# Performance work log

Hardware: AMD Instinct MI355X
Metric: run time of the kernel (lower is better)

Reference implementation:

```python
import jax, jax.numpy as jnp
import numpy as np

INPUT, HIDDEN, C, H, W, PK = 64, 128, 16, 32, 32, 4
B, T = 512, 1024

def hardsigmoid(v):
    return jnp.clip(v / 6.0 + 0.5, 0.0, 1.0)

def setup_inputs() -> dict:
    key = jax.random.key(0)
    ks = jax.random.split(key, 9)
    s_rnn = 1.0 / np.sqrt(HIDDEN)
    s_map = 1.0 / np.sqrt(HIDDEN)
    return {
        "x": jax.random.normal(ks[0], (B, T, INPUT), dtype=jnp.float32),
        "W_ih": jax.random.uniform(ks[1], (HIDDEN, INPUT), minval=-s_rnn, maxval=s_rnn),
        "b_ih": jax.random.uniform(ks[2], (HIDDEN,), minval=-s_rnn, maxval=s_rnn),
        "W_hh": jax.random.uniform(ks[3], (HIDDEN, HIDDEN), minval=-s_rnn, maxval=s_rnn),
        "b_hh": jax.random.uniform(ks[4], (HIDDEN,), minval=-s_rnn, maxval=s_rnn),
        "W_gate": jax.random.uniform(ks[5], (HIDDEN, HIDDEN), minval=-s_rnn, maxval=s_rnn),
        "b_gate": jax.random.uniform(ks[6], (HIDDEN,), minval=-s_rnn, maxval=s_rnn),
        "W_map": jax.random.uniform(ks[7], (C * H * W, HIDDEN), minval=-s_map, maxval=s_map),
        "b_map": jax.random.uniform(ks[8], (C * H * W,), minval=-s_map, maxval=s_map),
    }

def reference(x, W_ih, b_ih, W_hh, b_hh, W_gate, b_gate, W_map, b_map):
    batch, seq_len, _ = x.shape
    h0 = jnp.zeros((batch, HIDDEN), dtype=x.dtype)
    agg0 = jnp.zeros((batch, HIDDEN), dtype=x.dtype)

    def step(carry, xt):
        h, agg = carry
        h = jnp.tanh(xt @ W_ih.T + b_ih + h @ W_hh.T + b_hh)
        gate = hardsigmoid(h @ W_gate.T + b_gate)
        return (h, agg + h * gate), None

    (h, agg), _ = jax.lax.scan(step, (h0, agg0), jnp.swapaxes(x, 0, 1))
    agg = agg / float(seq_len)

    mapped = (agg @ W_map.T + b_map).reshape(batch, C, H, W)
    # AvgPool2d(kernel=PK, stride=PK) via reshape-mean
    pooled = mapped.reshape(batch, C, H // PK, PK, W // PK, PK).mean(axis=(3, 5))
    upsampled = jnp.repeat(jnp.repeat(pooled, PK, axis=2), PK, axis=3)
    return mapped * hardsigmoid(upsampled)
```

## Files before the change

kernel.cpp:

```cpp
#include <hip/hip_runtime.h>
#include <hip/hip_bf16.h>

#define T_SEQ 1024
#define BATCH 512
#define INPUT 64
#define HID   128

typedef __attribute__((ext_vector_type(8))) short bf16x8;
typedef __attribute__((ext_vector_type(4))) short s16x4;
typedef __attribute__((ext_vector_type(4))) float f32x4;
typedef __attribute__((ext_vector_type(2))) unsigned int u32x2;

#define MFMA __builtin_amdgcn_mfma_f32_16x16x32_bf16

__device__ __forceinline__ short f2bf(float f) {
    union { float f; unsigned u; } v; v.f = f;
    unsigned r = (v.u + 0x7FFFu + ((v.u >> 16) & 1u)) >> 16;
    return (short)r;
}

__device__ __forceinline__ unsigned cvtpk_bf16(float lo, float hi) {
    unsigned r;
    asm("v_cvt_pk_bf16_f32 %0, %1, %2" : "=v"(r) : "v"(lo), "v"(hi));
    return r;
}

__device__ __forceinline__ float fast_tanh(float s) {
    float e = __expf(2.0f * s);
    return 1.0f - 2.0f * __builtin_amdgcn_rcpf(e + 1.0f);
}

__device__ __forceinline__ float hsig(float v) {
    return __builtin_amdgcn_fmed3f(v * 0.16666666666666666f + 0.5f, 0.0f, 1.0f);
}

__device__ __forceinline__ void wg_barrier_lds() {
    asm volatile("s_waitcnt lgkmcnt(0)" ::: "memory");
    __builtin_amdgcn_s_barrier();
    asm volatile("" ::: "memory");
}

__global__ __launch_bounds__(256) void cvt_kernel(const float* __restrict__ in,
                                                  short* __restrict__ out, int n4) {
    int i = blockIdx.x * 256 + threadIdx.x;
    if (i >= n4) return;
    f32x4 v = ((const f32x4*)in)[i];
    s16x4 o;
    #pragma unroll
    for (int j = 0; j < 4; ++j) o[j] = f2bf(v[j]);
    ((s16x4*)out)[i] = o;
}

template<bool PRE>
__global__ __launch_bounds__(512, 2) void rnn_kernel(
    const float* __restrict__ xf_, const short* __restrict__ xb,
    const float* __restrict__ W_ih, const float* __restrict__ b_ih,
    const float* __restrict__ W_hh, const float* __restrict__ b_hh,
    const float* __restrict__ W_gate, const float* __restrict__ b_gate,
    float* __restrict__ agg_out)
{
    __shared__ __align__(16) short sh[2][16][136];

    const int tid  = threadIdx.x;
    const int wave = tid >> 6, lane = tid & 63;
    const int q = lane >> 4, l15 = lane & 15;
    const int b0 = blockIdx.x * 16;
    const int group = wave >> 2;
    const int gw = wave & 3;
    const int R0 = 32 * gw, R1 = R0 + 16;

    bf16x8 wih[2][2], whh[2][4], wgf[2][4];
    #pragma unroll
    for (int tile = 0; tile < 2; ++tile) {
        const int row = (tile ? R1 : R0) + l15;
        #pragma unroll
        for (int f = 0; f < 2; ++f) {
            const float* p = W_ih + row * INPUT + f * 32 + q * 8;
            bf16x8 v;
            #pragma unroll
            for (int j = 0; j < 8; ++j) v[j] = f2bf(p[j]);
            wih[tile][f] = v;
        }
        #pragma unroll
        for (int f = 0; f < 4; ++f) {
            const float* p = W_hh + row * HID + f * 32 + q * 8;
            bf16x8 v;
            #pragma unroll
            for (int j = 0; j < 8; ++j) v[j] = f2bf(p[j]);
            whh[tile][f] = v;
        }
        #pragma unroll
        for (int f = 0; f < 4; ++f) {
            const float* p = W_gate + row * HID + f * 32 + q * 8;
            bf16x8 v;
            #pragma unroll
            for (int j = 0; j < 8; ++j) v[j] = f2bf(p[j]);
            wgf[tile][f] = v;
        }
    }

    f32x4 bias1[2], biasg[2], zero4;
    #pragma unroll
    for (int tile = 0; tile < 2; ++tile) {
        const int rbase = (tile ? R1 : R0) + q * 4;
        #pragma unroll
        for (int r = 0; r < 4; ++r) {
            bias1[tile][r] = b_ih[rbase + r] + b_hh[rbase + r];
            biasg[tile][r] = b_gate[rbase + r];
        }
    }
    #pragma unroll
    for (int r = 0; r < 4; ++r) zero4[r] = 0.0f;

    f32x4 agg0 = zero4, agg1 = zero4;
    f32x4 hpA = zero4, hpB = zero4;
    f32x4 accx0, accx1;
    bf16x8 xf0, xf1;

    const long lanebase = ((long)(b0 + l15) * T_SEQ) * INPUT + q * 8;
    const short* xb_lane = PRE ? (xb + lanebase) : nullptr;
    const float* xf_lane = PRE ? nullptr : (xf_ + lanebase);

    auto load_x = [&](int tt) {
        if constexpr (PRE) {
            const short* p = xb_lane + (long)tt * INPUT;
            xf0 = *(const bf16x8*)p;
            xf1 = *(const bf16x8*)(p + 32);
        } else {
            const float* p = xf_lane + (long)tt * INPUT;
            f32x4 a0 = *(const f32x4*)p,        a1 = *(const f32x4*)(p + 4);
            f32x4 a2 = *(const f32x4*)(p + 32), a3 = *(const f32x4*)(p + 36);
            #pragma unroll
            for (int j = 0; j < 4; ++j) {
                xf0[j] = f2bf(a0[j]); xf0[4 + j] = f2bf(a1[j]);
                xf1[j] = f2bf(a2[j]); xf1[4 + j] = f2bf(a3[j]);
            }
        }
    };

    auto critical = [&](int t) {
        const int rb = (t & 1) ^ 1, wb = t & 1;
        bf16x8 hf0 = *(const bf16x8*)&sh[rb][l15][q * 8];
        bf16x8 hf1 = *(const bf16x8*)&sh[rb][l15][32 + q * 8];
        bf16x8 hf2 = *(const bf16x8*)&sh[rb][l15][64 + q * 8];
        bf16x8 hf3 = *(const bf16x8*)&sh[rb][l15][96 + q * 8];
        f32x4 a0 = MFMA(whh[0][0], hf0, accx0, 0, 0, 0);
        f32x4 c0 = MFMA(whh[0][2], hf2, zero4, 0, 0, 0);
        f32x4 a1 = MFMA(whh[1][0], hf0, accx1, 0, 0, 0);
        f32x4 c1 = MFMA(whh[1][2], hf2, zero4, 0, 0, 0);
        a0 = MFMA(whh[0][1], hf1, a0, 0, 0, 0);
        c0 = MFMA(whh[0][3], hf3, c0, 0, 0, 0);
        a1 = MFMA(whh[1][1], hf1, a1, 0, 0, 0);
        c1 = MFMA(whh[1][3], hf3, c1, 0, 0, 0);
        int tt = t + 2; if (tt > T_SEQ - 1) tt = T_SEQ - 1;
        load_x(tt);
        hpA[0] = fast_tanh(a0[0] + c0[0]);
        hpA[1] = fast_tanh(a0[1] + c0[1]);
        hpA[2] = fast_tanh(a0[2] + c0[2]);
        hpA[3] = fast_tanh(a0[3] + c0[3]);
        hpB[0] = fast_tanh(a1[0] + c1[0]);
        hpB[1] = fast_tanh(a1[1] + c1[1]);
        hpB[2] = fast_tanh(a1[2] + c1[2]);
        hpB[3] = fast_tanh(a1[3] + c1[3]);
        u32x2 p0, p1;
        p0[0] = cvtpk_bf16(hpA[0], hpA[1]); p0[1] = cvtpk_bf16(hpA[2], hpA[3]);
        p1[0] = cvtpk_bf16(hpB[0], hpB[1]); p1[1] = cvtpk_bf16(hpB[2], hpB[3]);
        *(u32x2*)&sh[wb][l15][R0 + q * 4] = p0;
        *(u32x2*)&sh[wb][l15][R1 + q * 4] = p1;
    };

    auto shadow = [&](int t) {
        const int rb = (t & 1) ^ 1;
        bf16x8 gf0 = *(const bf16x8*)&sh[rb][l15][q * 8];
        bf16x8 gf1 = *(const bf16x8*)&sh[rb][l15][32 + q * 8];
        bf16x8 gf2 = *(const bf16x8*)&sh[rb][l15][64 + q * 8];
        bf16x8 gf3 = *(const bf16x8*)&sh[rb][l15][96 + q * 8];
        f32x4 g0 = MFMA(wgf[0][0], gf0, biasg[0], 0, 0, 0);
        f32x4 e0 = MFMA(wgf[0][2], gf2, zero4, 0, 0, 0);
        f32x4 g1 = MFMA(wgf[1][0], gf0, biasg[1], 0, 0, 0);
        f32x4 e1 = MFMA(wgf[1][2], gf2, zero4, 0, 0, 0);
        g0 = MFMA(wgf[0][1], gf1, g0, 0, 0, 0);
        e0 = MFMA(wgf[0][3], gf3, e0, 0, 0, 0);
        g1 = MFMA(wgf[1][1], gf1, g1, 0, 0, 0);
        e1 = MFMA(wgf[1][3], gf3, e1, 0, 0, 0);
        accx0 = MFMA(wih[0][0], xf0, bias1[0], 0, 0, 0);
        accx1 = MFMA(wih[1][0], xf0, bias1[1], 0, 0, 0);
        accx0 = MFMA(wih[0][1], xf1, accx0, 0, 0, 0);
        accx1 = MFMA(wih[1][1], xf1, accx1, 0, 0, 0);
        #pragma unroll
        for (int r = 0; r < 4; ++r) {
            agg0[r] += hpA[r] * hsig(g0[r] + e0[r]);
            agg1[r] += hpB[r] * hsig(g1[r] + e1[r]);
        }
    };

    load_x(group);
    accx0 = MFMA(wih[0][0], xf0, bias1[0], 0, 0, 0);
    accx1 = MFMA(wih[1][0], xf0, bias1[1], 0, 0, 0);
    accx0 = MFMA(wih[0][1], xf1, accx0, 0, 0, 0);
    accx1 = MFMA(wih[1][1], xf1, accx1, 0, 0, 0);
    if (group == 0) {
        hpA[0] = fast_tanh(accx0[0]); hpA[1] = fast_tanh(accx0[1]);
        hpA[2] = fast_tanh(accx0[2]); hpA[3] = fast_tanh(accx0[3]);
        hpB[0] = fast_tanh(accx1[0]); hpB[1] = fast_tanh(accx1[1]);
        hpB[2] = fast_tanh(accx1[2]); hpB[3] = fast_tanh(accx1[3]);
        u32x2 p0, p1;
        p0[0] = cvtpk_bf16(hpA[0], hpA[1]); p0[1] = cvtpk_bf16(hpA[2], hpA[3]);
        p1[0] = cvtpk_bf16(hpB[0], hpB[1]); p1[1] = cvtpk_bf16(hpB[2], hpB[3]);
        *(u32x2*)&sh[0][l15][R0 + q * 4] = p0;
        *(u32x2*)&sh[0][l15][R1 + q * 4] = p1;
        load_x(2);
    }
    wg_barrier_lds();

    if (group == 0) {
        for (int i = 0; i < 511; ++i) {
            shadow(2 * i + 1);   wg_barrier_lds();
            critical(2 * i + 2); wg_barrier_lds();
        }
        shadow(1023); wg_barrier_lds();
    } else {
        for (int i = 0; i < 511; ++i) {
            critical(2 * i + 1); wg_barrier_lds();
            shadow(2 * i + 2);   wg_barrier_lds();
        }
        critical(1023); wg_barrier_lds();
    }

    if (group == 1) {
        bf16x8 gf0 = *(const bf16x8*)&sh[1][l15][q * 8];
        bf16x8 gf1 = *(const bf16x8*)&sh[1][l15][32 + q * 8];
        bf16x8 gf2 = *(const bf16x8*)&sh[1][l15][64 + q * 8];
        bf16x8 gf3 = *(const bf16x8*)&sh[1][l15][96 + q * 8];
        f32x4 g0 = MFMA(wgf[0][0], gf0, biasg[0], 0, 0, 0);
        f32x4 e0 = MFMA(wgf[0][2], gf2, zero4, 0, 0, 0);
        f32x4 g1 = MFMA(wgf[1][0], gf0, biasg[1], 0, 0, 0);
        f32x4 e1 = MFMA(wgf[1][2], gf2, zero4, 0, 0, 0);
        g0 = MFMA(wgf[0][1], gf1, g0, 0, 0, 0);
        e0 = MFMA(wgf[0][3], gf3, e0, 0, 0, 0);
        g1 = MFMA(wgf[1][1], gf1, g1, 0, 0, 0);
        e1 = MFMA(wgf[1][3], gf3, e1, 0, 0, 0);
        #pragma unroll
        for (int r = 0; r < 4; ++r) {
            agg0[r] += hpA[r] * hsig(g0[r] + e0[r]);
            agg1[r] += hpB[r] * hsig(g1[r] + e1[r]);
        }
    }
    wg_barrier_lds();

    float* aggf = (float*)&sh[0][0][0];
    if (group == 0) {
        *(f32x4*)&aggf[l15 * HID + R0 + q * 4] = agg0;
        *(f32x4*)&aggf[l15 * HID + R1 + q * 4] = agg1;
    }
    wg_barrier_lds();
    if (group == 1) {
        const float s = 1.0f / (float)T_SEQ;
        f32x4 t0 = *(const f32x4*)&aggf[l15 * HID + R0 + q * 4];
        f32x4 t1 = *(const f32x4*)&aggf[l15 * HID + R1 + q * 4];
        #pragma unroll
        for (int r = 0; r < 4; ++r) { t0[r] = (t0[r] + agg0[r]) * s; t1[r] = (t1[r] + agg1[r]) * s; }
        *(f32x4*)&agg_out[(long)(b0 + l15) * HID + R0 + q * 4] = t0;
        *(f32x4*)&agg_out[(long)(b0 + l15) * HID + R1 + q * 4] = t1;
    }
}

template<bool PRE>
__global__ __launch_bounds__(256) void map_kernel(
    const float* __restrict__ agg, const float* __restrict__ Wf,
    const short* __restrict__ Wb, const float* __restrict__ b_map,
    float* __restrict__ mapped)
{
    const int tid  = threadIdx.x;
    const int wave = tid >> 6, lane = tid & 63;
    const int q = lane >> 4, l15 = lane & 15;
    const int mb = blockIdx.x & 31;
    const int nb = blockIdx.x >> 5;
    const int b0 = mb * 16;
    const int n0 = nb * 128 + wave * 32;

    bf16x8 af[4];
    #pragma unroll
    for (int kb = 0; kb < 4; ++kb) {
        const float* p = agg + (b0 + l15) * HID + kb * 32 + q * 8;
        bf16x8 f;
        #pragma unroll
        for (int j = 0; j < 8; ++j) f[j] = f2bf(p[j]);
        af[kb] = f;
    }
    #pragma unroll
    for (int tn = 0; tn < 2; ++tn) {
        int nn = n0 + tn * 16 + l15;
        float bias = b_map[nn];
        f32x4 c;
        #pragma unroll
        for (int r = 0; r < 4; ++r) c[r] = bias;
        #pragma unroll
        for (int kb = 0; kb < 4; ++kb) {
            bf16x8 f;
            if (PRE) {
                f = *(const bf16x8*)(Wb + (long)nn * HID + kb * 32 + q * 8);
            } else {
                const float* p = Wf + (long)nn * HID + kb * 32 + q * 8;
                #pragma unroll
                for (int j = 0; j < 8; ++j) f[j] = f2bf(p[j]);
            }
            c = __builtin_amdgcn_mfma_f32_16x16x32_bf16(af[kb], f, c, 0, 0, 0);
        }
        #pragma unroll
        for (int r = 0; r < 4; ++r)
            mapped[(long)(b0 + q * 4 + r) * 16384 + nn] = c[r];
    }
}

__global__ __launch_bounds__(256) void pool_gate_kernel(float* __restrict__ mapped)
{
    __shared__ float sh_part[256];
    __shared__ float sh_gate[64];
    const int tid = threadIdx.x;
    float* plane = mapped + (long)blockIdx.x * 1024;

    f32x4 m4 = *(const f32x4*)(plane + tid * 4);
    sh_part[tid] = m4[0] + m4[1] + m4[2] + m4[3];
    __syncthreads();
    if (tid < 64) {
        int ph = tid >> 3, pw = tid & 7;
        float s = 0.0f;
        #pragma unroll
        for (int i = 0; i < 4; ++i) s += sh_part[(4 * ph + i) * 8 + pw];
        sh_gate[tid] = hsig(s * (1.0f / 16.0f));
    }
    __syncthreads();
    int h = tid >> 3, wb = tid & 7;
    float g = sh_gate[(h >> 2) * 8 + wb];
    f32x4 o = m4 * g;
    *(f32x4*)(plane + tid * 4) = o;
}

extern "C" void kernel_launch(void* const* d_in, const int* in_sizes, int n_in,
                              void* d_out, int out_size, void* d_ws, size_t ws_size,
                              hipStream_t stream) {
    const float* x      = (const float*)d_in[0];
    const float* W_ih   = (const float*)d_in[1];
    const float* b_ih   = (const float*)d_in[2];
    const float* W_hh   = (const float*)d_in[3];
    const float* b_hh   = (const float*)d_in[4];
    const float* W_gate = (const float*)d_in[5];
    const float* b_gate = (const float*)d_in[6];
    const float* W_map  = (const float*)d_in[7];
    const float* b_map  = (const float*)d_in[8];
    float* out = (float*)d_out;

    const size_t xb_bytes = (size_t)BATCH * T_SEQ * INPUT * 2;
    const size_t wm_bytes = (size_t)16384 * HID * 2;
    const size_t agg_bytes = (size_t)BATCH * HID * 4;
    const bool pre = ws_size >= xb_bytes + wm_bytes + agg_bytes;

    if (pre) {
        short* x_bf  = (short*)d_ws;
        short* wm_bf = (short*)((char*)d_ws + xb_bytes);
        float* agg   = (float*)((char*)d_ws + xb_bytes + wm_bytes);

        cvt_kernel<<<(BATCH * T_SEQ * INPUT / 4 + 255) / 256, 256, 0, stream>>>(x, x_bf, BATCH * T_SEQ * INPUT / 4);
        cvt_kernel<<<(16384 * HID / 4 + 255) / 256, 256, 0, stream>>>(W_map, wm_bf, 16384 * HID / 4);
        rnn_kernel<true><<<32, 512, 0, stream>>>(x, x_bf, W_ih, b_ih, W_hh, b_hh,
                                                 W_gate, b_gate, agg);
        map_kernel<true><<<4096, 256, 0, stream>>>(agg, W_map, wm_bf, b_map, out);
    } else {
        float* agg = (float*)d_ws;
        rnn_kernel<false><<<32, 512, 0, stream>>>(x, nullptr, W_ih, b_ih, W_hh, b_hh,
                                                  W_gate, b_gate, agg);
        map_kernel<false><<<4096, 256, 0, stream>>>(agg, W_map, nullptr, b_map, out);
    }
    pool_gate_kernel<<<BATCH * 16, 256, 0, stream>>>(out);
}
```

Measured before the change: 694.7 us.

## Merge RNN wave groups into one 256-thread block with software-pipelined gate and input

Before, the RNN kernel used two 4-wave groups that alternated critical (recurrent) and shadow (gate/input projection) phases with a barrier between each phase. Now a single 4-wave group does every step. Each step reads h once and issues the recurrent, gate and next-input MFMAs together. Gate application is delayed one step and x is prefetched three steps ahead. The goal is to halve barriers per timestep, drop the cross-group LDS reduction, and let independent MFMAs fill the latency of the serial tanh chain. The cost is more MFMA and VALU work on the critical path per wave, since the gate matmul no longer runs in a separate group.

After: 718.4 us. 1.03x slower.

```diff
diff --git a/kernel.cpp b/kernel.cpp
--- a/kernel.cpp
+++ b/kernel.cpp
@@ -52,7 +52,7 @@
 }
 
 template<bool PRE>
-__global__ __launch_bounds__(512, 2) void rnn_kernel(
+__global__ __launch_bounds__(256) void rnn_kernel(
     const float* __restrict__ xf_, const short* __restrict__ xb,
     const float* __restrict__ W_ih, const float* __restrict__ b_ih,
     const float* __restrict__ W_hh, const float* __restrict__ b_hh,
@@ -65,9 +65,7 @@
     const int wave = tid >> 6, lane = tid & 63;
     const int q = lane >> 4, l15 = lane & 15;
     const int b0 = blockIdx.x * 16;
-    const int group = wave >> 2;
-    const int gw = wave & 3;
-    const int R0 = 32 * gw, R1 = R0 + 16;
+    const int R0 = 32 * wave, R1 = R0 + 16;
 
     bf16x8 wih[2][2], whh[2][4], wgf[2][4];
     #pragma unroll
@@ -113,156 +111,145 @@
     for (int r = 0; r < 4; ++r) zero4[r] = 0.0f;
 
     f32x4 agg0 = zero4, agg1 = zero4;
-    f32x4 hpA = zero4, hpB = zero4;
-    f32x4 accx0, accx1;
-    bf16x8 xf0, xf1;
+    f32x4 hp1_0 = zero4, hp1_1 = zero4;
+    f32x4 hp2_0 = zero4, hp2_1 = zero4;
+    f32x4 gat0 = zero4, gat1 = zero4;
+    f32x4 axA0, axA1, axB0, axB1;
+    bf16x8 xB0a, xB0b, xB1a, xB1b;
 
     const long lanebase = ((long)(b0 + l15) * T_SEQ) * INPUT + q * 8;
     const short* xb_lane = PRE ? (xb + lanebase) : nullptr;
     const float* xf_lane = PRE ? nullptr : (xf_ + lanebase);
 
-    auto load_x = [&](int tt) {
+    auto load_pair = [&](int tt, bf16x8& fa, bf16x8& fb) {
         if constexpr (PRE) {
             const short* p = xb_lane + (long)tt * INPUT;
-            xf0 = *(const bf16x8*)p;
-            xf1 = *(const bf16x8*)(p + 32);
+            fa = *(const bf16x8*)p;
+            fb = *(const bf16x8*)(p + 32);
         } else {
             const float* p = xf_lane + (long)tt * INPUT;
             f32x4 a0 = *(const f32x4*)p,        a1 = *(const f32x4*)(p + 4);
             f32x4 a2 = *(const f32x4*)(p + 32), a3 = *(const f32x4*)(p + 36);
             #pragma unroll
             for (int j = 0; j < 4; ++j) {
-                xf0[j] = f2bf(a0[j]); xf0[4 + j] = f2bf(a1[j]);
-                xf1[j] = f2bf(a2[j]); xf1[4 + j] = f2bf(a3[j]);
+                fa[j] = f2bf(a0[j]); fa[4 + j] = f2bf(a1[j]);
+                fb[j] = f2bf(a2[j]); fb[4 + j] = f2bf(a3[j]);
             }
         }
     };
 
-    auto critical = [&](int t) {
+    auto step = [&](int t, f32x4& axM0, f32x4& axM1, f32x4& axS0, f32x4& axS1,
+                    bf16x8& xfa, bf16x8& xfb) {
         const int rb = (t & 1) ^ 1, wb = t & 1;
         bf16x8 hf0 = *(const bf16x8*)&sh[rb][l15][q * 8];
         bf16x8 hf1 = *(const bf16x8*)&sh[rb][l15][32 + q * 8];
         bf16x8 hf2 = *(const bf16x8*)&sh[rb][l15][64 + q * 8];
         bf16x8 hf3 = *(const bf16x8*)&sh[rb][l15][96 + q * 8];
-        f32x4 a0 = MFMA(whh[0][0], hf0, accx0, 0, 0, 0);
+        #pragma unroll
+        for (int r = 0; r < 4; ++r) {
+            agg0[r] += hp2_0[r] * hsig(gat0[r]);
+            agg1[r] += hp2_1[r] * hsig(gat1[r]);
+        }
+        axS0 = MFMA(wih[0][0], xfa, bias1[0], 0, 0, 0);
+        axS1 = MFMA(wih[1][0], xfa, bias1[1], 0, 0, 0);
+        axS0 = MFMA(wih[0][1], xfb, axS0, 0, 0, 0);
+        axS1 = MFMA(wih[1][1], xfb, axS1, 0, 0, 0);
+        int tt = t + 3; if (tt > T_SEQ - 1) tt = T_SEQ - 1;
+        load_pair(tt, xfa, xfb);
+        f32x4 a0 = MFMA(whh[0][0], hf0, axM0, 0, 0, 0);
         f32x4 c0 = MFMA(whh[0][2], hf2, zero4, 0, 0, 0);
-        f32x4 a1 = MFMA(whh[1][0], hf0, accx1, 0, 0, 0);
+        f32x4 a1 = MFMA(whh[1][0], hf0, axM1, 0, 0, 0);
         f32x4 c1 = MFMA(whh[1][2], hf2, zero4, 0, 0, 0);
         a0 = MFMA(whh[0][1], hf1, a0, 0, 0, 0);
         c0 = MFMA(whh[0][3], hf3, c0, 0, 0, 0);
         a1 = MFMA(whh[1][1], hf1, a1, 0, 0, 0);
         c1 = MFMA(whh[1][3], hf3, c1, 0, 0, 0);
-        int tt = t + 2; if (tt > T_SEQ - 1) tt = T_SEQ - 1;
-        load_x(tt);
-        hpA[0] = fast_tanh(a0[0] + c0[0]);
-        hpA[1] = fast_tanh(a0[1] + c0[1]);
-        hpA[2] = fast_tanh(a0[2] + c0[2]);
-        hpA[3] = fast_tanh(a0[3] + c0[3]);
-        hpB[0] = fast_tanh(a1[0] + c1[0]);
-        hpB[1] = fast_tanh(a1[1] + c1[1]);
-        hpB[2] = fast_tanh(a1[2] + c1[2]);
-        hpB[3] = fast_tanh(a1[3] + c1[3]);
+        gat0 = MFMA(wgf[0][0], hf0, biasg[0], 0, 0, 0);
+        gat0 = MFMA(wgf[0][1], hf1, gat0, 0, 0, 0);
+        gat0 = MFMA(wgf[0][2], hf2, gat0, 0, 0, 0);
+        gat0 = MFMA(wgf[0][3], hf3, gat0, 0, 0, 0);
+        gat1 = MFMA(wgf[1][0], hf0, biasg[1], 0, 0, 0);
+        gat1 = MFMA(wgf[1][1], hf1, gat1, 0, 0, 0);
+        gat1 = MFMA(wgf[1][2], hf2, gat1, 0, 0, 0);
+        gat1 = MFMA(wgf[1][3], hf3, gat1, 0, 0, 0);
+        hp2_0 = hp1_0; hp2_1 = hp1_1;
+        hp1_0[0] = fast_tanh(a0[0] + c0[0]);
+        hp1_0[1] = fast_tanh(a0[1] + c0[1]);
+        hp1_0[2] = fast_tanh(a0[2] + c0[2]);
+        hp1_0[3] = fast_tanh(a0[3] + c0[3]);
+        hp1_1[0] = fast_tanh(a1[0] + c1[0]);
+        hp1_1[1] = fast_tanh(a1[1] + c1[1]);
+        hp1_1[2] = fast_tanh(a1[2] + c1[2]);
+        hp1_1[3] = fast_tanh(a1[3] + c1[3]);
         u32x2 p0, p1;
-        p0[0] = cvtpk_bf16(hpA[0], hpA[1]); p0[1] = cvtpk_bf16(hpA[2], hpA[3]);
-        p1[0] = cvtpk_bf16(hpB[0], hpB[1]); p1[1] = cvtpk_bf16(hpB[2], hpB[3]);
+        p0[0] = cvtpk_bf16(hp1_0[0], hp1_0[1]); p0[1] = cvtpk_bf16(hp1_0[2], hp1_0[3]);
+        p1[0] = cvtpk_bf16(hp1_1[0], hp1_1[1]); p1[1] = cvtpk_bf16(hp1_1[2], hp1_1[3]);
         *(u32x2*)&sh[wb][l15][R0 + q * 4] = p0;
         *(u32x2*)&sh[wb][l15][R1 + q * 4] = p1;
+        wg_barrier_lds();
     };
 
-    auto shadow = [&](int t) {
-        const int rb = (t & 1) ^ 1;
-        bf16x8 gf0 = *(const bf16x8*)&sh[rb][l15][q * 8];
-        bf16x8 gf1 = *(const bf16x8*)&sh[rb][l15][32 + q * 8];
-        bf16x8 gf2 = *(const bf16x8*)&sh[rb][l15][64 + q * 8];
-        bf16x8 gf3 = *(const bf16x8*)&sh[rb][l15][96 + q * 8];
-        f32x4 g0 = MFMA(wgf[0][0], gf0, biasg[0], 0, 0, 0);
-        f32x4 e0 = MFMA(wgf[0][2], gf2, zero4, 0, 0, 0);
-        f32x4 g1 = MFMA(wgf[1][0], gf0, biasg[1], 0, 0, 0);
-        f32x4 e1 = MFMA(wgf[1][2], gf2, zero4, 0, 0, 0);
-        g0 = MFMA(wgf[0][1], gf1, g0, 0, 0, 0);
-        e0 = MFMA(wgf[0][3], gf3, e0, 0, 0, 0);
-        g1 = MFMA(wgf[1][1], gf1, g1, 0, 0, 0);
-        e1 = MFMA(wgf[1][3], gf3, e1, 0, 0, 0);
-        accx0 = MFMA(wih[0][0], xf0, bias1[0], 0, 0, 0);
-        accx1 = MFMA(wih[1][0], xf0, bias1[1], 0, 0, 0);
-        accx0 = MFMA(wih[0][1], xf1, accx0, 0, 0, 0);
-        accx1 = MFMA(wih[1][1], xf1, accx1, 0, 0, 0);
-        #pragma unroll
-        for (int r = 0; r < 4; ++r) {
-            agg0[r] += hpA[r] * hsig(g0[r] + e0[r]);
-            agg1[r] += hpB[r] * hsig(g1[r] + e1[r]);
-        }
-    };
-
-    load_x(group);
-    accx0 = MFMA(wih[0][0], xf0, bias1[0], 0, 0, 0);
-    accx1 = MFMA(wih[1][0], xf0, bias1[1], 0, 0, 0);
-    accx0 = MFMA(wih[0][1], xf1, accx0, 0, 0, 0);
-    accx1 = MFMA(wih[1][1], xf1, accx1, 0, 0, 0);
-    if (group == 0) {
-        hpA[0] = fast_tanh(accx0[0]); hpA[1] = fast_tanh(accx0[1]);
-        hpA[2] = fast_tanh(accx0[2]); hpA[3] = fast_tanh(accx0[3]);
-        hpB[0] = fast_tanh(accx1[0]); hpB[1] = fast_tanh(accx1[1]);
-        hpB[2] = fast_tanh(accx1[2]); hpB[3] = fast_tanh(accx1[3]);
+    {
+        bf16x8 ta, tb;
+        load_pair(0, ta, tb);
+        axA0 = MFMA(wih[0][0], ta, bias1[0], 0, 0, 0);
+        axA1 = MFMA(wih[1][0], ta, bias1[1], 0, 0, 0);
+        axA0 = MFMA(wih[0][1], tb, axA0, 0, 0, 0);
+        axA1 = MFMA(wih[1][1], tb, axA1, 0, 0, 0);
+        hp1_0[0] = fast_tanh(axA0[0]); hp1_0[1] = fast_tanh(axA0[1]);
+        hp1_0[2] = fast_tanh(axA0[2]); hp1_0[3] = fast_tanh(axA0[3]);
+        hp1_1[0] = fast_tanh(axA1[0]); hp1_1[1] = fast_tanh(axA1[1]);
+        hp1_1[2] = fast_tanh(axA1[2]); hp1_1[3] = fast_tanh(axA1[3]);
         u32x2 p0, p1;
-        p0[0] = cvtpk_bf16(hpA[0], hpA[1]); p0[1] = cvtpk_bf16(hpA[2], hpA[3]);
-        p1[0] = cvtpk_bf16(hpB[0], hpB[1]); p1[1] = cvtpk_bf16(hpB[2], hpB[3]);
+        p0[0] = cvtpk_bf16(hp1_0[0], hp1_0[1]); p0[1] = cvtpk_bf16(hp1_0[2], hp1_0[3]);
+        p1[0] = cvtpk_bf16(hp1_1[0], hp1_1[1]); p1[1] = cvtpk_bf16(hp1_1[2], hp1_1[3]);
         *(u32x2*)&sh[0][l15][R0 + q * 4] = p0;
         *(u32x2*)&sh[0][l15][R1 + q * 4] = p1;
-        load_x(2);
-    }
-    wg_barrier_lds();
-
-    if (group == 0) {
-        for (int i = 0; i < 511; ++i) {
-            shadow(2 * i + 1);   wg_barrier_lds();
-            critical(2 * i + 2); wg_barrier_lds();
-        }
-        shadow(1023); wg_barrier_lds();
-    } else {
-        for (int i = 0; i < 511; ++i) {
-            critical(2 * i + 1); wg_barrier_lds();
-            shadow(2 * i + 2);   wg_barrier_lds();
-        }
-        critical(1023); wg_barrier_lds();
-    }
-
-    if (group == 1) {
-        bf16x8 gf0 = *(const bf16x8*)&sh[1][l15][q * 8];
-        bf16x8 gf1 = *(const bf16x8*)&sh[1][l15][32 + q * 8];
-        bf16x8 gf2 = *(const bf16x8*)&sh[1][l15][64 + q * 8];
-        bf16x8 gf3 = *(const bf16x8*)&sh[1][l15][96 + q * 8];
-        f32x4 g0 = MFMA(wgf[0][0], gf0, biasg[0], 0, 0, 0);
-        f32x4 e0 = MFMA(wgf[0][2], gf2, zero4, 0, 0, 0);
-        f32x4 g1 = MFMA(wgf[1][0], gf0, biasg[1], 0, 0, 0);
-        f32x4 e1 = MFMA(wgf[1][2], gf2, zero4, 0, 0, 0);
-        g0 = MFMA(wgf[0][1], gf1, g0, 0, 0, 0);
-        e0 = MFMA(wgf[0][3], gf3, e0, 0, 0, 0);
-        g1 = MFMA(wgf[1][1], gf1, g1, 0, 0, 0);
-        e1 = MFMA(wgf[1][3], gf3, e1, 0, 0, 0);
+        load_pair(1, ta, tb);
+        axA0 = MFMA(wih[0][0], ta, bias1[0], 0, 0, 0);
+        axA1 = MFMA(wih[1][0], ta, bias1[1], 0, 0, 0);
+        axA0 = MFMA(wih[0][1], tb, axA0, 0, 0, 0);
+        axA1 = MFMA(wih[1][1], tb, axA1, 0, 0, 0);
+        load_pair(2, xB0a, xB0b);
+        load_pair(3, xB1a, xB1b);
+        wg_barrier_lds();
+    }
+
+    for (int i = 0; i < 511; ++i) {
+        step(2 * i + 1, axA0, axA1, axB0, axB1, xB0a, xB0b);
+        step(2 * i + 2, axB0, axB1, axA0, axA1, xB1a, xB1b);
+    }
+    step(1023, axA0, axA1, axB0, axB1, xB0a, xB0b);
+
+    #pragma unroll
+    for (int r = 0; r < 4; ++r) {
+        agg0[r] += hp2_0[r] * hsig(gat0[r]);
+        agg1[r] += hp2_1[r] * hsig(gat1[r]);
+    }
+    {
+        bf16x8 hf0 = *(const bf16x8*)&sh[1][l15][q * 8];
+        bf16x8 hf1 = *(const bf16x8*)&sh[1][l15][32 + q * 8];
+        bf16x8 hf2 = *(const bf16x8*)&sh[1][l15][64 + q * 8];
+        bf16x8 hf3 = *(const bf16x8*)&sh[1][l15][96 + q * 8];
+        gat0 = MFMA(wgf[0][0], hf0, biasg[0], 0, 0, 0);
+        gat0 = MFMA(wgf[0][1], hf1, gat0, 0, 0, 0);
+        gat0 = MFMA(wgf[0][2], hf2, gat0, 0, 0, 0);
+        gat0 = MFMA(wgf[0][3], hf3, gat0, 0, 0, 0);
+        gat1 = MFMA(wgf[1][0], hf0, biasg[1], 0, 0, 0);
+        gat1 = MFMA(wgf[1][1], hf1, gat1, 0, 0, 0);
+        gat1 = MFMA(wgf[1][2], hf2, gat1, 0, 0, 0);
+        gat1 = MFMA(wgf[1][3], hf3, gat1, 0, 0, 0);
         #pragma unroll
         for (int r = 0; r < 4; ++r) {
-            agg0[r] += hpA[r] * hsig(g0[r] + e0[r]);
-            agg1[r] += hpB[r] * hsig(g1[r] + e1[r]);
-        }
-    }
-    wg_barrier_lds();
-
-    float* aggf = (float*)&sh[0][0][0];
-    if (group == 0) {
-        *(f32x4*)&aggf[l15 * HID + R0 + q * 4] = agg0;
-        *(f32x4*)&aggf[l15 * HID + R1 + q * 4] = agg1;
-    }
-    wg_barrier_lds();
-    if (group == 1) {
-        const float s = 1.0f / (float)T_SEQ;
-        f32x4 t0 = *(const f32x4*)&aggf[l15 * HID + R0 + q * 4];
-        f32x4 t1 = *(const f32x4*)&aggf[l15 * HID + R1 + q * 4];
-        #pragma unroll
-        for (int r = 0; r < 4; ++r) { t0[r] = (t0[r] + agg0[r]) * s; t1[r] = (t1[r] + agg1[r]) * s; }
-        *(f32x4*)&agg_out[(long)(b0 + l15) * HID + R0 + q * 4] = t0;
-        *(f32x4*)&agg_out[(long)(b0 + l15) * HID + R1 + q * 4] = t1;
-    }
+            agg0[r] += hp1_0[r] * hsig(gat0[r]);
+            agg1[r] += hp1_1[r] * hsig(gat1[r]);
+        }
+    }
+    const float s = 1.0f / (float)T_SEQ;
+    #pragma unroll
+    for (int r = 0; r < 4; ++r) { agg0[r] *= s; agg1[r] *= s; }
+    *(f32x4*)&agg_out[(long)(b0 + l15) * HID + R0 + q * 4] = agg0;
+    *(f32x4*)&agg_out[(long)(b0 + l15) * HID + R1 + q * 4] = agg1;
 }
 
 template<bool PRE>
@@ -363,12 +350,12 @@
 
         cvt_kernel<<<(BATCH * T_SEQ * INPUT / 4 + 255) / 256, 256, 0, stream>>>(x, x_bf, BATCH * T_SEQ * INPUT / 4);
         cvt_kernel<<<(16384 * HID / 4 + 255) / 256, 256, 0, stream>>>(W_map, wm_bf, 16384 * HID / 4);
-        rnn_kernel<true><<<32, 512, 0, stream>>>(x, x_bf, W_ih, b_ih, W_hh, b_hh,
+        rnn_kernel<true><<<32, 256, 0, stream>>>(x, x_bf, W_ih, b_ih, W_hh, b_hh,
                                                  W_gate, b_gate, agg);
         map_kernel<true><<<4096, 256, 0, stream>>>(agg, W_map, wm_bf, b_map, out);
     } else {
         float* agg = (float*)d_ws;
-        rnn_kernel<false><<<32, 512, 0, stream>>>(x, nullptr, W_ih, b_ih, W_hh, b_hh,
+        rnn_kernel<false><<<32, 256, 0, stream>>>(x, nullptr, W_ih, b_ih, W_hh, b_hh,
                                                   W_gate, b_gate, agg);
         map_kernel<false><<<4096, 256, 0, stream>>>(agg, W_map, nullptr, b_map, out);
     }
```

## Drop x bf16 pre-conversion, prefetch fp32 x deeper, fuse pool-gate into map kernel

Applied to the files above, without the earlier changes.

Removes the separate kernel that converted the full input sequence to bf16. The RNN kernel now loads fp32 x directly into a double-buffered register prefetch several steps ahead, converting it inside the shadow phase. It also folds the 4x4 average-pool and hardsigmoid gating into the map kernel using shuffles and shared memory, which eliminates the extra read and write pass over the output tensor. The cost is more registers (launch bounds changed to 1 block per SM) and in-loop conversion work on the recurrent path.

New measurement: 769.2 us. 10.7% more time.

```diff
diff --git a/kernel.cpp b/kernel.cpp
--- a/kernel.cpp
+++ b/kernel.cpp
@@ -51,9 +51,8 @@
     ((s16x4*)out)[i] = o;
 }
 
-template<bool PRE>
-__global__ __launch_bounds__(512, 2) void rnn_kernel(
-    const float* __restrict__ xf_, const short* __restrict__ xb,
+__global__ __launch_bounds__(512, 1) void rnn_kernel(
+    const float* __restrict__ xf_,
     const float* __restrict__ W_ih, const float* __restrict__ b_ih,
     const float* __restrict__ W_hh, const float* __restrict__ b_hh,
     const float* __restrict__ W_gate, const float* __restrict__ b_gate,
@@ -115,28 +114,9 @@
     f32x4 agg0 = zero4, agg1 = zero4;
     f32x4 hpA = zero4, hpB = zero4;
     f32x4 accx0, accx1;
-    bf16x8 xf0, xf1;
-
-    const long lanebase = ((long)(b0 + l15) * T_SEQ) * INPUT + q * 8;
-    const short* xb_lane = PRE ? (xb + lanebase) : nullptr;
-    const float* xf_lane = PRE ? nullptr : (xf_ + lanebase);
-
-    auto load_x = [&](int tt) {
-        if constexpr (PRE) {
-            const short* p = xb_lane + (long)tt * INPUT;
-            xf0 = *(const bf16x8*)p;
-            xf1 = *(const bf16x8*)(p + 32);
-        } else {
-            const float* p = xf_lane + (long)tt * INPUT;
-            f32x4 a0 = *(const f32x4*)p,        a1 = *(const f32x4*)(p + 4);
-            f32x4 a2 = *(const f32x4*)(p + 32), a3 = *(const f32x4*)(p + 36);
-            #pragma unroll
-            for (int j = 0; j < 4; ++j) {
-                xf0[j] = f2bf(a0[j]); xf0[4 + j] = f2bf(a1[j]);
-                xf1[j] = f2bf(a2[j]); xf1[4 + j] = f2bf(a3[j]);
-            }
-        }
-    };
+    f32x4 P0, P1, P2, P3, Q0, Q1, Q2, Q3;
+
+    const float* xf_lane = xf_ + ((long)(b0 + l15) * T_SEQ) * INPUT + q * 8;
 
     auto critical = [&](int t) {
         const int rb = (t & 1) ^ 1, wb = t & 1;
@@ -152,8 +132,6 @@
         c0 = MFMA(whh[0][3], hf3, c0, 0, 0, 0);
         a1 = MFMA(whh[1][1], hf1, a1, 0, 0, 0);
         c1 = MFMA(whh[1][3], hf3, c1, 0, 0, 0);
-        int tt = t + 2; if (tt > T_SEQ - 1) tt = T_SEQ - 1;
-        load_x(tt);
         hpA[0] = fast_tanh(a0[0] + c0[0]);
         hpA[1] = fast_tanh(a0[1] + c0[1]);
         hpA[2] = fast_tanh(a0[2] + c0[2]);
@@ -169,12 +147,28 @@
         *(u32x2*)&sh[wb][l15][R1 + q * 4] = p1;
     };
 
-    auto shadow = [&](int t) {
+    auto shadow = [&](int t, f32x4& r0, f32x4& r1, f32x4& r2, f32x4& r3) {
         const int rb = (t & 1) ^ 1;
         bf16x8 gf0 = *(const bf16x8*)&sh[rb][l15][q * 8];
         bf16x8 gf1 = *(const bf16x8*)&sh[rb][l15][32 + q * 8];
         bf16x8 gf2 = *(const bf16x8*)&sh[rb][l15][64 + q * 8];
         bf16x8 gf3 = *(const bf16x8*)&sh[rb][l15][96 + q * 8];
+        bf16x8 fa, fb;
+        #pragma unroll
+        for (int j = 0; j < 4; ++j) {
+            fa[j] = f2bf(r0[j]); fa[4 + j] = f2bf(r1[j]);
+            fb[j] = f2bf(r2[j]); fb[4 + j] = f2bf(r3[j]);
+        }
+        accx0 = MFMA(wih[0][0], fa, bias1[0], 0, 0, 0);
+        accx1 = MFMA(wih[1][0], fa, bias1[1], 0, 0, 0);
+        accx0 = MFMA(wih[0][1], fb, accx0, 0, 0, 0);
+        accx1 = MFMA(wih[1][1], fb, accx1, 0, 0, 0);
+        int tt = t + 5; if (tt > T_SEQ - 1) tt = T_SEQ - 1;
+        {
+            const float* p = xf_lane + (long)tt * INPUT;
+            r0 = *(const f32x4*)p;        r1 = *(const f32x4*)(p + 4);
+            r2 = *(const f32x4*)(p + 32); r3 = *(const f32x4*)(p + 36);
+        }
         f32x4 g0 = MFMA(wgf[0][0], gf0, biasg[0], 0, 0, 0);
         f32x4 e0 = MFMA(wgf[0][2], gf2, zero4, 0, 0, 0);
         f32x4 g1 = MFMA(wgf[1][0], gf0, biasg[1], 0, 0, 0);
@@ -183,10 +177,6 @@
         e0 = MFMA(wgf[0][3], gf3, e0, 0, 0, 0);
         g1 = MFMA(wgf[1][1], gf1, g1, 0, 0, 0);
         e1 = MFMA(wgf[1][3], gf3, e1, 0, 0, 0);
-        accx0 = MFMA(wih[0][0], xf0, bias1[0], 0, 0, 0);
-        accx1 = MFMA(wih[1][0], xf0, bias1[1], 0, 0, 0);
-        accx0 = MFMA(wih[0][1], xf1, accx0, 0, 0, 0);
-        accx1 = MFMA(wih[1][1], xf1, accx1, 0, 0, 0);
         #pragma unroll
         for (int r = 0; r < 4; ++r) {
             agg0[r] += hpA[r] * hsig(g0[r] + e0[r]);
@@ -194,35 +184,58 @@
         }
     };
 
-    load_x(group);
-    accx0 = MFMA(wih[0][0], xf0, bias1[0], 0, 0, 0);
-    accx1 = MFMA(wih[1][0], xf0, bias1[1], 0, 0, 0);
-    accx0 = MFMA(wih[0][1], xf1, accx0, 0, 0, 0);
-    accx1 = MFMA(wih[1][1], xf1, accx1, 0, 0, 0);
+    {
+        const float* p = xf_lane + (long)group * INPUT;
+        f32x4 a0 = *(const f32x4*)p,        a1 = *(const f32x4*)(p + 4);
+        f32x4 a2 = *(const f32x4*)(p + 32), a3 = *(const f32x4*)(p + 36);
+        bf16x8 ta, tb;
+        #pragma unroll
+        for (int j = 0; j < 4; ++j) {
+            ta[j] = f2bf(a0[j]); ta[4 + j] = f2bf(a1[j]);
+            tb[j] = f2bf(a2[j]); tb[4 + j] = f2bf(a3[j]);
+        }
+        accx0 = MFMA(wih[0][0], ta, bias1[0], 0, 0, 0);
+        accx1 = MFMA(wih[1][0], ta, bias1[1], 0, 0, 0);
+        accx0 = MFMA(wih[0][1], tb, accx0, 0, 0, 0);
+        accx1 = MFMA(wih[1][1], tb, accx1, 0, 0, 0);
+        if (group == 0) {
+            hpA[0] = fast_tanh(accx0[0]); hpA[1] = fast_tanh(accx0[1]);
+            hpA[2] = fast_tanh(accx0[2]); hpA[3] = fast_tanh(accx0[3]);
+            hpB[0] = fast_tanh(accx1[0]); hpB[1] = fast_tanh(accx1[1]);
+            hpB[2] = fast_tanh(accx1[2]); hpB[3] = fast_tanh(accx1[3]);
+            u32x2 p0, p1;
+            p0[0] = cvtpk_bf16(hpA[0], hpA[1]); p0[1] = cvtpk_bf16(hpA[2], hpA[3]);
+            p1[0] = cvtpk_bf16(hpB[0], hpB[1]); p1[1] = cvtpk_bf16(hpB[2], hpB[3]);
+            *(u32x2*)&sh[0][l15][R0 + q * 4] = p0;
+            *(u32x2*)&sh[0][l15][R1 + q * 4] = p1;
+        }
+        const float* pp = xf_lane + (long)(group ? 3 : 2) * INPUT;
+        P0 = *(const f32x4*)pp;        P1 = *(const f32x4*)(pp + 4);
+        P2 = *(const f32x4*)(pp + 32); P3 = *(const f32x4*)(pp + 36);
+        const float* pq = xf_lane + (long)(group ? 5 : 4) * INPUT;
+        Q0 = *(const f32x4*)pq;        Q1 = *(const f32x4*)(pq + 4);
+        Q2 = *(const f32x4*)(pq + 32); Q3 = *(const f32x4*)(pq + 36);
+    }
+    wg_barrier_lds();
+
     if (group == 0) {
-        hpA[0] = fast_tanh(accx0[0]); hpA[1] = fast_tanh(accx0[1]);
-        hpA[2] = fast_tanh(accx0[2]); hpA[3] = fast_tanh(accx0[3]);
-        hpB[0] = fast_tanh(accx1[0]); hpB[1] = fast_tanh(accx1[1]);
-        hpB[2] = fast_tanh(accx1[2]); hpB[3] = fast_tanh(accx1[3]);
-        u32x2 p0, p1;
-        p0[0] = cvtpk_bf16(hpA[0], hpA[1]); p0[1] = cvtpk_bf16(hpA[2], hpA[3]);
-        p1[0] = cvtpk_bf16(hpB[0], hpB[1]); p1[1] = cvtpk_bf16(hpB[2], hpB[3]);
-        *(u32x2*)&sh[0][l15][R0 + q * 4] = p0;
-        *(u32x2*)&sh[0][l15][R1 + q * 4] = p1;
-        load_x(2);
-    }
-    wg_barrier_lds();
-
-    if (group == 0) {
-        for (int i = 0; i < 511; ++i) {
-            shadow(2 * i + 1);   wg_barrier_lds();
-            critical(2 * i + 2); wg_barrier_lds();
-        }
-        shadow(1023); wg_barrier_lds();
+        shadow(1, P0, P1, P2, P3);   wg_barrier_lds();
+        critical(2);                 wg_barrier_lds();
+        for (int i = 0; i < 255; ++i) {
+            shadow(4 * i + 3, Q0, Q1, Q2, Q3); wg_barrier_lds();
+            critical(4 * i + 4);               wg_barrier_lds();
+            shadow(4 * i + 5, P0, P1, P2, P3); wg_barrier_lds();
+            critical(4 * i + 6);               wg_barrier_lds();
+        }
+        shadow(1023, Q0, Q1, Q2, Q3); wg_barrier_lds();
     } else {
-        for (int i = 0; i < 511; ++i) {
-            critical(2 * i + 1); wg_barrier_lds();
-            shadow(2 * i + 2);   wg_barrier_lds();
+        critical(1);                 wg_barrier_lds();
+        shadow(2, P0, P1, P2, P3);   wg_barrier_lds();
+        for (int i = 0; i < 255; ++i) {
+            critical(4 * i + 3);               wg_barrier_lds();
+            shadow(4 * i + 4, Q0, Q1, Q2, Q3); wg_barrier_lds();
+            critical(4 * i + 5);               wg_barrier_lds();
+            shadow(4 * i + 6, P0, P1, P2, P3); wg_barrier_lds();
         }
         critical(1023); wg_barrier_lds();
     }
@@ -269,8 +282,11 @@
 __global__ __launch_bounds__(256) void map_kernel(
     const float* __restrict__ agg, const float* __restrict__ Wf,
     const short* __restrict__ Wb, const float* __restrict__ b_map,
-    float* __restrict__ mapped)
+    float* __restrict__ out)
 {
+    __shared__ float sh_pool[4][16][8];
+    __shared__ float sh_gate[16][8];
+
     const int tid  = threadIdx.x;
     const int wave = tid >> 6, lane = tid & 63;
     const int q = lane >> 4, l15 = lane & 15;
@@ -288,6 +304,7 @@
         for (int j = 0; j < 8; ++j) f[j] = f2bf(p[j]);
         af[kb] = f;
     }
+    f32x4 cc[2];
     #pragma unroll
     for (int tn = 0; tn < 2; ++tn) {
         int nn = n0 + tn * 16 + l15;
@@ -307,34 +324,35 @@
             }
             c = __builtin_amdgcn_mfma_f32_16x16x32_bf16(af[kb], f, c, 0, 0, 0);
         }
+        cc[tn] = c;
+        f32x4 t = c;
+        #pragma unroll
+        for (int r = 0; r < 4; ++r) {
+            t[r] += __shfl_xor(t[r], 1);
+            t[r] += __shfl_xor(t[r], 2);
+        }
+        if ((l15 & 3) == 0) {
+            int pw = tn * 4 + (l15 >> 2);
+            #pragma unroll
+            for (int r = 0; r < 4; ++r) sh_pool[wave][q * 4 + r][pw] = t[r];
+        }
+    }
+    __syncthreads();
+    if (tid < 128) {
+        int b = tid >> 3, pw = tid & 7;
+        float s = sh_pool[0][b][pw] + sh_pool[1][b][pw] +
+                  sh_pool[2][b][pw] + sh_pool[3][b][pw];
+        sh_gate[b][pw] = hsig(s * (1.0f / 16.0f));
+    }
+    __syncthreads();
+    #pragma unroll
+    for (int tn = 0; tn < 2; ++tn) {
+        int nn = n0 + tn * 16 + l15;
+        int pw = tn * 4 + (l15 >> 2);
         #pragma unroll
         for (int r = 0; r < 4; ++r)
-            mapped[(long)(b0 + q * 4 + r) * 16384 + nn] = c[r];
-    }
-}
-
-__global__ __launch_bounds__(256) void pool_gate_kernel(float* __restrict__ mapped)
-{
-    __shared__ float sh_part[256];
-    __shared__ float sh_gate[64];
-    const int tid = threadIdx.x;
-    float* plane = mapped + (long)blockIdx.x * 1024;
-
-    f32x4 m4 = *(const f32x4*)(plane + tid * 4);
-    sh_part[tid] = m4[0] + m4[1] + m4[2] + m4[3];
-    __syncthreads();
-    if (tid < 64) {
-        int ph = tid >> 3, pw = tid & 7;
-        float s = 0.0f;
-        #pragma unroll
-        for (int i = 0; i < 4; ++i) s += sh_part[(4 * ph + i) * 8 + pw];
-        sh_gate[tid] = hsig(s * (1.0f / 16.0f));
-    }
-    __syncthreads();
-    int h = tid >> 3, wb = tid & 7;
-    float g = sh_gate[(h >> 2) * 8 + wb];
-    f32x4 o = m4 * g;
-    *(f32x4*)(plane + tid * 4) = o;
+            out[(long)(b0 + q * 4 + r) * 16384 + nn] = cc[tn][r] * sh_gate[q * 4 + r][pw];
+    }
 }
 
 extern "C" void kernel_launch(void* const* d_in, const int* in_sizes, int n_in,
@@ -351,26 +369,22 @@
     const float* b_map  = (const float*)d_in[8];
     float* out = (float*)d_out;
 
-    const size_t xb_bytes = (size_t)BATCH * T_SEQ * INPUT * 2;
     const size_t wm_bytes = (size_t)16384 * HID * 2;
     const size_t agg_bytes = (size_t)BATCH * HID * 4;
-    const bool pre = ws_size >= xb_bytes + wm_bytes + agg_bytes;
+    const bool pre = ws_size >= wm_bytes + agg_bytes;
 
     if (pre) {
-        short* x_bf  = (short*)d_ws;
-        short* wm_bf = (short*)((char*)d_ws + xb_bytes);
-        float* agg   = (float*)((char*)d_ws + xb_bytes + wm_bytes);
-
-        cvt_kernel<<<(BATCH * T_SEQ * INPUT / 4 + 255) / 256, 256, 0, stream>>>(x, x_bf, BATCH * T_SEQ * INPUT / 4);
+        short* wm_bf = (short*)d_ws;
+        float* agg   = (float*)((char*)d_ws + wm_bytes);
+
         cvt_kernel<<<(16384 * HID / 4 + 255) / 256, 256, 0, stream>>>(W_map, wm_bf, 16384 * HID / 4);
-        rnn_kernel<true><<<32, 512, 0, stream>>>(x, x_bf, W_ih, b_ih, W_hh, b_hh,
-                                                 W_gate, b_gate, agg);
+        rnn_kernel<<<32, 512, 0, stream>>>(x, W_ih, b_ih, W_hh, b_hh,
+                                           W_gate, b_gate, agg);
         map_kernel<true><<<4096, 256, 0, stream>>>(agg, W_map, wm_bf, b_map, out);
     } else {
         float* agg = (float*)d_ws;
-        rnn_kernel<false><<<32, 512, 0, stream>>>(x, nullptr, W_ih, b_ih, W_hh, b_hh,
-                                                  W_gate, b_gate, agg);
+        rnn_kernel<<<32, 512, 0, stream>>>(x, W_ih, b_ih, W_hh, b_hh,
+                                           W_gate, b_gate, agg);
         map_kernel<false><<<4096, 256, 0, stream>>>(agg, W_map, nullptr, b_map, out);
     }
-    pool_gate_kernel<<<BATCH * 16, 256, 0, stream>>>(out);
-}
+}
```

## Fuse avg-pool gating into map GEMM epilogue and split recurrent MFMA chains

Applied to the files above, without the earlier changes.

Removes the separate pool_gate kernel. The map kernel now computes the 4x4 pooled means in its epilogue using lane shuffles and shared memory, then writes the gated output directly. This avoids re-reading and re-writing the full 32 MB mapped tensor, at the cost of two block barriers in the map kernel. Separately, the recurrent step's MFMA accumulation is split into four independent chains summed at the end, which shortens the dependent MFMA latency on the critical serial path.

After: 702.3 us. About the same (+1.1%).

```diff
diff --git a/kernel.cpp b/kernel.cpp
--- a/kernel.cpp
+++ b/kernel.cpp
@@ -145,23 +145,25 @@
         bf16x8 hf2 = *(const bf16x8*)&sh[rb][l15][64 + q * 8];
         bf16x8 hf3 = *(const bf16x8*)&sh[rb][l15][96 + q * 8];
         f32x4 a0 = MFMA(whh[0][0], hf0, accx0, 0, 0, 0);
+        f32x4 a1 = MFMA(whh[1][0], hf0, accx1, 0, 0, 0);
+        f32x4 b0v = MFMA(whh[0][1], hf1, zero4, 0, 0, 0);
+        f32x4 b1v = MFMA(whh[1][1], hf1, zero4, 0, 0, 0);
         f32x4 c0 = MFMA(whh[0][2], hf2, zero4, 0, 0, 0);
-        f32x4 a1 = MFMA(whh[1][0], hf0, accx1, 0, 0, 0);
         f32x4 c1 = MFMA(whh[1][2], hf2, zero4, 0, 0, 0);
-        a0 = MFMA(whh[0][1], hf1, a0, 0, 0, 0);
-        c0 = MFMA(whh[0][3], hf3, c0, 0, 0, 0);
-        a1 = MFMA(whh[1][1], hf1, a1, 0, 0, 0);
-        c1 = MFMA(whh[1][3], hf3, c1, 0, 0, 0);
+        f32x4 d0 = MFMA(whh[0][3], hf3, zero4, 0, 0, 0);
+        f32x4 d1 = MFMA(whh[1][3], hf3, zero4, 0, 0, 0);
         int tt = t + 2; if (tt > T_SEQ - 1) tt = T_SEQ - 1;
         load_x(tt);
-        hpA[0] = fast_tanh(a0[0] + c0[0]);
-        hpA[1] = fast_tanh(a0[1] + c0[1]);
-        hpA[2] = fast_tanh(a0[2] + c0[2]);
-        hpA[3] = fast_tanh(a0[3] + c0[3]);
-        hpB[0] = fast_tanh(a1[0] + c1[0]);
-        hpB[1] = fast_tanh(a1[1] + c1[1]);
-        hpB[2] = fast_tanh(a1[2] + c1[2]);
-        hpB[3] = fast_tanh(a1[3] + c1[3]);
+        f32x4 s0 = (a0 + b0v) + (c0 + d0);
+        f32x4 s1 = (a1 + b1v) + (c1 + d1);
+        hpA[0] = fast_tanh(s0[0]);
+        hpA[1] = fast_tanh(s0[1]);
+        hpA[2] = fast_tanh(s0[2]);
+        hpA[3] = fast_tanh(s0[3]);
+        hpB[0] = fast_tanh(s1[0]);
+        hpB[1] = fast_tanh(s1[1]);
+        hpB[2] = fast_tanh(s1[2]);
+        hpB[3] = fast_tanh(s1[3]);
         u32x2 p0, p1;
         p0[0] = cvtpk_bf16(hpA[0], hpA[1]); p0[1] = cvtpk_bf16(hpA[2], hpA[3]);
         p1[0] = cvtpk_bf16(hpB[0], hpB[1]); p1[1] = cvtpk_bf16(hpB[2], hpB[3]);
@@ -269,8 +271,11 @@
 __global__ __launch_bounds__(256) void map_kernel(
     const float* __restrict__ agg, const float* __restrict__ Wf,
     const short* __restrict__ Wb, const float* __restrict__ b_map,
-    float* __restrict__ mapped)
+    float* __restrict__ out)
 {
+    __shared__ float sh_pool[4][16][8];
+    __shared__ float sh_gate[16][8];
+
     const int tid  = threadIdx.x;
     const int wave = tid >> 6, lane = tid & 63;
     const int q = lane >> 4, l15 = lane & 15;
@@ -288,6 +293,7 @@
         for (int j = 0; j < 8; ++j) f[j] = f2bf(p[j]);
         af[kb] = f;
     }
+    f32x4 cc[2];
     #pragma unroll
     for (int tn = 0; tn < 2; ++tn) {
         int nn = n0 + tn * 16 + l15;
@@ -307,34 +313,35 @@
             }
             c = __builtin_amdgcn_mfma_f32_16x16x32_bf16(af[kb], f, c, 0, 0, 0);
         }
+        cc[tn] = c;
+        f32x4 t = c;
+        #pragma unroll
+        for (int r = 0; r < 4; ++r) {
+            t[r] += __shfl_xor(t[r], 1);
+            t[r] += __shfl_xor(t[r], 2);
+        }
+        if ((l15 & 3) == 0) {
+            int pw = tn * 4 + (l15 >> 2);
+            #pragma unroll
+            for (int r = 0; r < 4; ++r) sh_pool[wave][q * 4 + r][pw] = t[r];
+        }
+    }
+    __syncthreads();
+    if (tid < 128) {
+        int b = tid >> 3, pw = tid & 7;
+        float s = sh_pool[0][b][pw] + sh_pool[1][b][pw] +
+                  sh_pool[2][b][pw] + sh_pool[3][b][pw];
+        sh_gate[b][pw] = hsig(s * (1.0f / 16.0f));
+    }
+    __syncthreads();
+    #pragma unroll
+    for (int tn = 0; tn < 2; ++tn) {
+        int nn = n0 + tn * 16 + l15;
+        int pw = tn * 4 + (l15 >> 2);
         #pragma unroll
         for (int r = 0; r < 4; ++r)
-            mapped[(long)(b0 + q * 4 + r) * 16384 + nn] = c[r];
-    }
-}
-
-__global__ __launch_bounds__(256) void pool_gate_kernel(float* __restrict__ mapped)
-{
-    __shared__ float sh_part[256];
-    __shared__ float sh_gate[64];
-    const int tid = threadIdx.x;
-    float* plane = mapped + (long)blockIdx.x * 1024;
-
-    f32x4 m4 = *(const f32x4*)(plane + tid * 4);
-    sh_part[tid] = m4[0] + m4[1] + m4[2] + m4[3];
-    __syncthreads();
-    if (tid < 64) {
-        int ph = tid >> 3, pw = tid & 7;
-        float s = 0.0f;
-        #pragma unroll
-        for (int i = 0; i < 4; ++i) s += sh_part[(4 * ph + i) * 8 + pw];
-        sh_gate[tid] = hsig(s * (1.0f / 16.0f));
-    }
-    __syncthreads();
-    int h = tid >> 3, wb = tid & 7;
-    float g = sh_gate[(h >> 2) * 8 + wb];
-    f32x4 o = m4 * g;
-    *(f32x4*)(plane + tid * 4) = o;
+            out[(long)(b0 + q * 4 + r) * 16384 + nn] = cc[tn][r] * sh_gate[q * 4 + r][pw];
+    }
 }
 
 extern "C" void kernel_launch(void* const* d_in, const int* in_sizes, int n_in,
@@ -372,5 +379,4 @@
                                                   W_gate, b_gate, agg);
         map_kernel<false><<<4096, 256, 0, stream>>>(agg, W_map, nullptr, b_map, out);
     }
-    pool_gate_kernel<<<BATCH * 16, 256, 0, stream>>>(out);
-}
+}
```
